# Performance work log

Measured on AMD Instinct MI355X. Metric: run time of the kernel, lower is better.

## Reference

```python
import jax, jax.numpy as jnp
import numpy as np

N_GROUPS = 40
MAX_DISPARITY = 48


def _groupwise(l, r, n_groups):
    # l, r: (N, C, H, W') -> (N, G, H, W') mean over channels within each group
    n, c, h, w = l.shape
    return (l * r).reshape(n, n_groups, c // n_groups, h, w).mean(axis=2)


def setup_inputs() -> dict:
    key = jax.random.key(0)
    k1, k2 = jax.random.split(key)
    left = jax.random.normal(k1, (4, 320, 80, 160), dtype=jnp.float32)
    right = jax.random.normal(k2, (4, 320, 80, 160), dtype=jnp.float32)
    return {"left": left, "right": right}


def reference(left, right):
    # Output: (N, n_groups, H, W, max_disparity) cost volume.
    n, c, h, w = left.shape
    slices = []
    for d in range(MAX_DISPARITY):  # static, small, structurally distinct shifts
        if d == 0:
            cost = _groupwise(left, right, N_GROUPS)
        else:
            cost = _groupwise(left[:, :, :, d:], right[:, :, :, : w - d], N_GROUPS)
            cost = jnp.pad(cost, ((0, 0), (0, 0), (0, 0), (d, 0)))  # zeros where w < d
        slices.append(cost)
    return jnp.stack(slices, axis=-1)
```

## Files before the change

kernel.cpp:

```cpp
#include <hip/hip_runtime.h>

typedef float f4 __attribute__((ext_vector_type(4)));

constexpr int N_  = 4;
constexpr int C_  = 320;
constexpr int H_  = 80;
constexpr int W_  = 160;
constexpr int G_  = 40;
constexpr int CPG = 8;
constexpr int D_  = 48;
constexpr int HW  = H_ * W_;
constexpr int QW  = 40;
constexpr int NQ  = W_ / QW;
constexpr int PADW = 48;
constexpr int RWN  = PADW + QW;
constexpr int TPW  = (QW / 4) * (D_ / 4);

__global__ __launch_bounds__(256) void gw_cost_kernel(const float* __restrict__ Lg,
                                                      const float* __restrict__ Rg,
                                                      float* __restrict__ out) {
    __shared__ float Ls[4][CPG][QW];
    __shared__ float Rs[4][CPG][RWN];

    const int tid  = threadIdx.x;
    const int wid  = tid >> 6;
    const int lane = tid & 63;

    const int task = blockIdx.x * 4 + wid;
    const int q    = task & (NQ - 1);
    const int row  = task >> 2;
    const int h = row % H_;
    const int g = (row / H_) % G_;
    const int n = row / (H_ * G_);
    const int w0q = q * QW;

    const size_t base = (size_t)(n * C_ + g * CPG) * HW + (size_t)h * W_;

    const int zl = (q == 0) ? PADW : (q == 1 ? 8 : 0);

    if (lane * 4 < zl) {
        #pragma unroll
        for (int c = 0; c < CPG; ++c)
            *(f4*)&Rs[wid][c][lane * 4] = (f4)(0.0f);
    }

    const int goffR = w0q - PADW + zl;
    const int nlR   = (RWN - zl) / 4;
    #pragma unroll
    for (int c = 0; c < CPG; ++c) {
        if (lane < QW / 4) {
            const float* gl = Lg + base + (size_t)c * HW + w0q + lane * 4;
            __builtin_amdgcn_global_load_lds(
                (const __attribute__((address_space(1))) void*)gl,
                (__attribute__((address_space(3))) void*)&Ls[wid][c][0], 16, 0, 0);
        }
        if (lane < nlR) {
            const float* gr = Rg + base + (size_t)c * HW + goffR + lane * 4;
            __builtin_amdgcn_global_load_lds(
                (const __attribute__((address_space(1))) void*)gr,
                (__attribute__((address_space(3))) void*)&Rs[wid][c][zl], 16, 0, 0);
        }
    }
    asm volatile("s_waitcnt vmcnt(0)" ::: "memory");
    __builtin_amdgcn_sched_barrier(0);

    for (int t = lane; t < TPW; t += 64) {
        const int twl = t / 12;
        const int td  = t % 12;
        const int w0l = twl * 4;
        const int d0  = td * 4;
        const int r0  = w0l - d0 + PADW;

        f4 a0 = (f4)(0.0f), a1 = (f4)(0.0f), a2 = (f4)(0.0f), a3 = (f4)(0.0f);

        #pragma unroll
        for (int c = 0; c < CPG; ++c) {
            const f4 lv = *(const f4*)&Ls[wid][c][w0l];
            const float* rp = &Rs[wid][c][r0 - 4];
            const f4 ra = *(const f4*)(rp);
            const f4 rb = *(const f4*)(rp + 4);
            float rr[8];
            #pragma unroll
            for (int k = 0; k < 4; ++k) { rr[k] = ra[k]; rr[4 + k] = rb[k]; }
            #pragma unroll
            for (int j = 0; j < 4; ++j) {
                a0[j] += lv[0] * rr[4 + 0 - j];
                a1[j] += lv[1] * rr[4 + 1 - j];
                a2[j] += lv[2] * rr[4 + 2 - j];
                a3[j] += lv[3] * rr[4 + 3 - j];
            }
        }

        float* op = out + (size_t)row * (W_ * D_) + (size_t)(w0q + w0l) * D_ + d0;
        *(f4*)(op + 0 * D_) = a0 * 0.125f;
        *(f4*)(op + 1 * D_) = a1 * 0.125f;
        *(f4*)(op + 2 * D_) = a2 * 0.125f;
        *(f4*)(op + 3 * D_) = a3 * 0.125f;
    }
}

extern "C" void kernel_launch(void* const* d_in, const int* in_sizes, int n_in,
                              void* d_out, int out_size, void* d_ws, size_t ws_size,
                              hipStream_t stream) {
    const float* Lg = (const float*)d_in[0];
    const float* Rg = (const float*)d_in[1];
    float* out = (float*)d_out;

    const int nblocks = (N_ * G_ * H_ * NQ) / 4;
    gw_cost_kernel<<<dim3(nblocks), dim3(256), 0, stream>>>(Lg, Rg, out);
}
```

Measured before the change: 117.3 us.

## Use persistent blocks with double-buffered async LDS loads over half-row chunks

Replaces the one-shot grid (four independent quarter-row tasks per block) with a persistent grid of 2048 blocks. Each block loops over half-row chunks and double-buffers the global-to-LDS loads, so the next chunk's input transfer overlaps the current chunk's compute. Each block now cooperates on one 80-wide half row: every wave loads two channels, and 240 of 256 threads compute. This adds per-iteration block barriers and reshapes the R halo handling, in exchange for hiding load latency and cutting redundant halo loads.

Result: no change. 116.4 us (-0.8%).

```diff
diff --git a/kernel.cpp b/kernel.cpp
--- a/kernel.cpp
+++ b/kernel.cpp
@@ -10,92 +10,104 @@
 constexpr int CPG = 8;
 constexpr int D_  = 48;
 constexpr int HW  = H_ * W_;
-constexpr int QW  = 40;
-constexpr int NQ  = W_ / QW;
-constexpr int PADW = 48;
-constexpr int RWN  = PADW + QW;
-constexpr int TPW  = (QW / 4) * (D_ / 4);
+constexpr int ROWS   = N_ * G_ * H_;
+constexpr int CHUNKS = ROWS * 2;
+constexpr int NBLK   = 2048;
+constexpr int HALF   = 80;
+constexpr int TPC    = (HALF / 4) * (D_ / 4);
 
 __global__ __launch_bounds__(256) void gw_cost_kernel(const float* __restrict__ Lg,
                                                       const float* __restrict__ Rg,
                                                       float* __restrict__ out) {
-    __shared__ float Ls[4][CPG][QW];
-    __shared__ float Rs[4][CPG][RWN];
+    __shared__ float Lsh[2][CPG][HALF];
+    __shared__ float Rsh[2][CPG][128];
 
     const int tid  = threadIdx.x;
     const int wid  = tid >> 6;
     const int lane = tid & 63;
+    const int bid  = blockIdx.x;
+    const int par  = bid & 1;
+    const int c0   = wid * 2;
 
-    const int task = blockIdx.x * 4 + wid;
-    const int q    = task & (NQ - 1);
-    const int row  = task >> 2;
-    const int h = row % H_;
-    const int g = (row / H_) % G_;
-    const int n = row / (H_ * G_);
-    const int w0q = q * QW;
-
-    const size_t base = (size_t)(n * C_ + g * CPG) * HW + (size_t)h * W_;
-
-    const int zl = (q == 0) ? PADW : (q == 1 ? 8 : 0);
-
-    if (lane * 4 < zl) {
-        #pragma unroll
-        for (int c = 0; c < CPG; ++c)
-            *(f4*)&Rs[wid][c][lane * 4] = (f4)(0.0f);
+    if (par == 0 && tid < 2 * CPG * 12) {
+        const int b = tid / 96, q = tid % 96, c = q / 12, p = q % 12;
+        *(f4*)&Rsh[b][c][p * 4] = (f4)(0.0f);
     }
 
-    const int goffR = w0q - PADW + zl;
-    const int nlR   = (RWN - zl) / 4;
-    #pragma unroll
-    for (int c = 0; c < CPG; ++c) {
-        if (lane < QW / 4) {
-            const float* gl = Lg + base + (size_t)c * HW + w0q + lane * 4;
+    const int roff = par ? 0 : 48;
+    const int gw0  = par ? 32 : 0;
+    const int nlR  = par ? 32 : 20;
+
+    const int nch = (CHUNKS - bid + NBLK - 1) / NBLK;
+
+    const int w0l = (tid / 12) * 4;
+    const int d0  = (tid % 12) * 4;
+    const int r0l = w0l - d0 + 48;
+
+    auto issue = [&](int k) {
+        const int ch = bid + k * NBLK;
+        const int r  = ch >> 1;
+        const size_t base = (size_t)(r / H_) * (CPG * HW) + (size_t)(r % H_) * W_;
+        if (lane < 40) {
+            const int cc = c0 + lane / 20, wq = (lane % 20) * 4;
+            const float* s = Lg + base + (size_t)cc * HW + par * HALF + wq;
             __builtin_amdgcn_global_load_lds(
-                (const __attribute__((address_space(1))) void*)gl,
-                (__attribute__((address_space(3))) void*)&Ls[wid][c][0], 16, 0, 0);
+                (const __attribute__((address_space(1))) void*)s,
+                (__attribute__((address_space(3))) void*)&Lsh[k & 1][c0][0], 16, 0, 0);
         }
         if (lane < nlR) {
-            const float* gr = Rg + base + (size_t)c * HW + goffR + lane * 4;
+            const float* s0 = Rg + base + (size_t)c0 * HW + gw0 + lane * 4;
             __builtin_amdgcn_global_load_lds(
-                (const __attribute__((address_space(1))) void*)gr,
-                (__attribute__((address_space(3))) void*)&Rs[wid][c][zl], 16, 0, 0);
+                (const __attribute__((address_space(1))) void*)s0,
+                (__attribute__((address_space(3))) void*)&Rsh[k & 1][c0][roff], 16, 0, 0);
+            const float* s1 = Rg + base + (size_t)(c0 + 1) * HW + gw0 + lane * 4;
+            __builtin_amdgcn_global_load_lds(
+                (const __attribute__((address_space(1))) void*)s1,
+                (__attribute__((address_space(3))) void*)&Rsh[k & 1][c0 + 1][roff], 16, 0, 0);
         }
-    }
+    };
+
+    issue(0);
     asm volatile("s_waitcnt vmcnt(0)" ::: "memory");
-    __builtin_amdgcn_sched_barrier(0);
 
-    for (int t = lane; t < TPW; t += 64) {
-        const int twl = t / 12;
-        const int td  = t % 12;
-        const int w0l = twl * 4;
-        const int d0  = td * 4;
-        const int r0  = w0l - d0 + PADW;
+    for (int k = 0; k < nch; ++k) {
+        asm volatile("s_waitcnt vmcnt(4) lgkmcnt(0)" ::: "memory");
+        __builtin_amdgcn_s_barrier();
+        __builtin_amdgcn_sched_barrier(0);
 
-        f4 a0 = (f4)(0.0f), a1 = (f4)(0.0f), a2 = (f4)(0.0f), a3 = (f4)(0.0f);
+        if (k + 1 < nch) issue(k + 1);
 
-        #pragma unroll
-        for (int c = 0; c < CPG; ++c) {
-            const f4 lv = *(const f4*)&Ls[wid][c][w0l];
-            const float* rp = &Rs[wid][c][r0 - 4];
-            const f4 ra = *(const f4*)(rp);
-            const f4 rb = *(const f4*)(rp + 4);
-            float rr[8];
+        const int ch = bid + k * NBLK;
+        const int r  = ch >> 1;
+        const float (*Lp)[HALF] = Lsh[k & 1];
+        const float (*Rp)[128]  = Rsh[k & 1];
+
+        if (tid < TPC) {
+            f4 a0 = (f4)(0.f), a1 = (f4)(0.f), a2 = (f4)(0.f), a3 = (f4)(0.f);
             #pragma unroll
-            for (int k = 0; k < 4; ++k) { rr[k] = ra[k]; rr[4 + k] = rb[k]; }
-            #pragma unroll
-            for (int j = 0; j < 4; ++j) {
-                a0[j] += lv[0] * rr[4 + 0 - j];
-                a1[j] += lv[1] * rr[4 + 1 - j];
-                a2[j] += lv[2] * rr[4 + 2 - j];
-                a3[j] += lv[3] * rr[4 + 3 - j];
+            for (int c = 0; c < CPG; ++c) {
+                const f4 lv = *(const f4*)&Lp[c][w0l];
+                const float* rp = &Rp[c][r0l - 4];
+                const f4 ra = *(const f4*)rp;
+                const f4 rb = *(const f4*)(rp + 4);
+                float rr[8];
+                #pragma unroll
+                for (int t = 0; t < 4; ++t) { rr[t] = ra[t]; rr[4 + t] = rb[t]; }
+                #pragma unroll
+                for (int j = 0; j < 4; ++j) {
+                    a0[j] += lv[0] * rr[4 + 0 - j];
+                    a1[j] += lv[1] * rr[4 + 1 - j];
+                    a2[j] += lv[2] * rr[4 + 2 - j];
+                    a3[j] += lv[3] * rr[4 + 3 - j];
+                }
             }
+            float* op = out + (size_t)r * (W_ * D_)
+                        + (size_t)(par * HALF + w0l) * D_ + d0;
+            *(f4*)(op + 0 * D_) = a0 * 0.125f;
+            *(f4*)(op + 1 * D_) = a1 * 0.125f;
+            *(f4*)(op + 2 * D_) = a2 * 0.125f;
+            *(f4*)(op + 3 * D_) = a3 * 0.125f;
         }
-
-        float* op = out + (size_t)row * (W_ * D_) + (size_t)(w0q + w0l) * D_ + d0;
-        *(f4*)(op + 0 * D_) = a0 * 0.125f;
-        *(f4*)(op + 1 * D_) = a1 * 0.125f;
-        *(f4*)(op + 2 * D_) = a2 * 0.125f;
-        *(f4*)(op + 3 * D_) = a3 * 0.125f;
     }
 }
 
@@ -106,6 +118,5 @@
     const float* Rg = (const float*)d_in[1];
     float* out = (float*)d_out;
 
-    const int nblocks = (N_ * G_ * H_ * NQ) / 4;
-    gw_cost_kernel<<<dim3(nblocks), dim3(256), 0, stream>>>(Lg, Rg, out);
+    gw_cost_kernel<<<dim3(NBLK), dim3(256), 0, stream>>>(Lg, Rg, out);
 }
```
